# Kernel optimization log

Hardware: AMD Instinct MI355X
Metric: run time of the kernel (lower is better)

The kernel has to match this reference:

```python
import jax, jax.numpy as jnp
import numpy as np

D = 256; DFF = 1024; NH = 8; NL = 4; NP = 4; HD = D // NH
N = 8; LQ = 1024
SHAPES = np.array([[8, 64, 64], [8, 32, 32], [8, 16, 16], [8, 8, 8]], dtype=np.int32)
LIN = int(SHAPES.prod(axis=1).sum())  # 43520
LSI = np.concatenate([[0], np.cumsum(SHAPES.prod(axis=1))[:-1]]).astype(np.int32)


def setup_inputs() -> dict:
    key = jax.random.key(0)
    ks = jax.random.split(key, 16)
    s = 0.02
    inp = {
        "tgt": jax.random.normal(ks[0], (N, LQ, D), jnp.float32),
        "query_pos": jax.random.normal(ks[1], (N, LQ, D), jnp.float32),
        "reference_points": jax.random.uniform(ks[2], (N, LQ, NL, 3), jnp.float32),
        "src": jax.random.normal(ks[3], (N, LIN, D), jnp.float32),
        "src_spatio_temporal_shapes": jnp.asarray(SHAPES),
        "level_start_index": jnp.asarray(LSI),
        "src_padding_mask": jnp.zeros((N, LIN), dtype=bool),
        # MSDeformAttn3D params (weights stored (in,out) so y = x @ W + b)
        "value_proj_w": jax.random.normal(ks[4], (D, D), jnp.float32) * s,
        "value_proj_b": jnp.zeros((D,), jnp.float32),
        "samp_off_w": jax.random.normal(ks[5], (D, NH * NL * NP * 3), jnp.float32) * s,
        "samp_off_b": jax.random.normal(ks[6], (NH * NL * NP * 3,), jnp.float32) * s,
        "attn_w_w": jax.random.normal(ks[7], (D, NH * NL * NP), jnp.float32) * s,
        "attn_w_b": jnp.zeros((NH * NL * NP,), jnp.float32),
        "out_proj_w": jax.random.normal(ks[8], (D, D), jnp.float32) * s,
        "out_proj_b": jnp.zeros((D,), jnp.float32),
        # norm1 / FFN / norm3
        "ln1_g": jnp.ones((D,), jnp.float32),
        "ln1_b": jnp.zeros((D,), jnp.float32),
        "lin1_w": jax.random.normal(ks[9], (D, DFF), jnp.float32) * s,
        "lin1_b": jnp.zeros((DFF,), jnp.float32),
        "lin2_w": jax.random.normal(ks[10], (DFF, D), jnp.float32) * s,
        "lin2_b": jnp.zeros((D,), jnp.float32),
        "ln3_g": jnp.ones((D,), jnp.float32),
        "ln3_b": jnp.zeros((D,), jnp.float32),
    }
    return inp


def _ln(x, g, b, eps=1e-5):
    m = x.mean(-1, keepdims=True)
    v = x.var(-1, keepdims=True)
    return (x - m) / jnp.sqrt(v + eps) * g + b


def _ms_deform_attn3d(q, reference_points, src, shapes, lsi, pad_mask,
                      value_proj_w, value_proj_b, samp_off_w, samp_off_b,
                      attn_w_w, attn_w_b, out_proj_w, out_proj_b):
    n, lq, _ = q.shape
    value = src @ value_proj_w + value_proj_b                 # [N,Lin,D]
    value = jnp.where(pad_mask[:, :, None], 0.0, value)
    value = value.reshape(n, -1, NH, HD)                      # [N,Lin,H,hd]
    off = (q @ samp_off_w + samp_off_b).reshape(n, lq, NH, NL, NP, 3)
    aw = (q @ attn_w_w + attn_w_b).reshape(n, lq, NH, NL * NP)
    aw = jax.nn.softmax(aw, axis=-1).reshape(n, lq, NH, NL, NP)

    acc = jnp.zeros((n, lq, NH, HD), q.dtype)
    for l in range(NL):
        Tl, Hl, Wl = shapes[l, 0], shapes[l, 1], shapes[l, 2]
        sz = shapes[l].astype(q.dtype)                        # (T,H,W)
        start = lsi[l]
        # sampling locations in normalized (t,h,w) coords, [N,Lq,H,P,3]
        loc = reference_points[:, :, None, l, None, :] + off[:, :, :, l] / sz
        p = loc * sz - 0.5                                    # align_corners=False pixel coords
        p0 = jnp.floor(p)
        f = p - p0
        p0 = p0.astype(jnp.int32)
        samp = jnp.zeros((n, lq, NH, NP, HD), q.dtype)
        for dt in (0, 1):
            for dy in (0, 1):
                for dx in (0, 1):
                    it = p0[..., 0] + dt
                    iy = p0[..., 1] + dy
                    ix = p0[..., 2] + dx
                    w = ((f[..., 0] if dt else 1 - f[..., 0]) *
                         (f[..., 1] if dy else 1 - f[..., 1]) *
                         (f[..., 2] if dx else 1 - f[..., 2]))
                    valid = ((it >= 0) & (it < Tl) & (iy >= 0) & (iy < Hl) &
                             (ix >= 0) & (ix < Wl))
                    idx = start + (jnp.clip(it, 0, Tl - 1) * Hl +
                                   jnp.clip(iy, 0, Hl - 1)) * Wl + jnp.clip(ix, 0, Wl - 1)
                    # gather: idx [N,Lq,H,P] -> [N,Lq*P,H,1]
                    gi = idx.transpose(0, 1, 3, 2).reshape(n, lq * NP, NH, 1)
                    g = jnp.take_along_axis(value, gi, axis=1)
                    g = g.reshape(n, lq, NP, NH, HD).transpose(0, 1, 3, 2, 4)
                    samp = samp + (w * valid)[..., None] * g
        acc = acc + jnp.einsum('nqhp,nqhpd->nqhd', aw[:, :, :, l], samp)
    return acc.reshape(n, lq, D) @ out_proj_w + out_proj_b


def reference(tgt, query_pos, reference_points, src, src_spatio_temporal_shapes,
              level_start_index, src_padding_mask,
              value_proj_w, value_proj_b, samp_off_w, samp_off_b,
              attn_w_w, attn_w_b, out_proj_w, out_proj_b,
              ln1_g, ln1_b, lin1_w, lin1_b, lin2_w, lin2_b, ln3_g, ln3_b):
    q = tgt + query_pos
    tgt2 = _ms_deform_attn3d(q, reference_points, src, src_spatio_temporal_shapes,
                             level_start_index, src_padding_mask,
                             value_proj_w, value_proj_b, samp_off_w, samp_off_b,
                             attn_w_w, attn_w_b, out_proj_w, out_proj_b)
    x = _ln(tgt + tgt2, ln1_g, ln1_b)
    ff = jax.nn.relu(x @ lin1_w + lin1_b) @ lin2_w + lin2_b
    return _ln(x + ff, ln3_g, ln3_b)
```

## Files before the change

### kernel.cpp

```cpp
#include <hip/hip_runtime.h>

#define D_      256
#define DFF_    1024
#define NHEADS  8
#define NLVL    4
#define NPTS    4
#define HDIM    32
#define NBATCH  8
#define LQ_     1024
#define LIN_    43520
#define NQ_     (NBATCH * LQ_)
#define MV_     (NBATCH * LIN_)

typedef unsigned short u16;
typedef __attribute__((ext_vector_type(8))) short bf16x8;
typedef __attribute__((ext_vector_type(4))) float f32x4;

__device__ __forceinline__ u16 f2bf(float f) {
    unsigned u = __float_as_uint(f);
    return (u16)((u + 0x7FFFu + ((u >> 16) & 1u)) >> 16);
}
__device__ __forceinline__ float bf2f(u16 s) {
    return __uint_as_float(((unsigned)s) << 16);
}

template<bool OUT_BF16, bool RELU>
__global__ __launch_bounds__(256)
void gemm64(const float* __restrict__ A, const u16* __restrict__ Bt,
            const float* __restrict__ bias1, const float* __restrict__ bias2, int bsplit,
            const float* __restrict__ res,
            float* __restrict__ Cf, u16* __restrict__ Cb,
            int M, int N, int K)
{
    __shared__ u16 As[64][72];
    __shared__ u16 Bs[64][72];

    const int tid  = threadIdx.x;
    const int lane = tid & 63;
    const int w    = tid >> 6;
    const int wm   = w >> 1, wn = w & 1;
    const size_t m0 = (size_t)blockIdx.x * 64;
    const int    n0 = blockIdx.y * 64;
    const int r15 = lane & 15;
    const int kq  = lane >> 4;

    const f32x4 zero = {0.f, 0.f, 0.f, 0.f};
    f32x4 acc[2][2] = {{zero, zero}, {zero, zero}};

    for (int kt = 0; kt < K; kt += 64) {
        #pragma unroll
        for (int i = 0; i < 4; ++i) {
            int f   = tid + i * 256;
            int row = f >> 4;
            int c4  = f & 15;
            float4 v = *(const float4*)(A + (m0 + row) * K + kt + c4 * 4);
            unsigned lo = (unsigned)f2bf(v.x) | ((unsigned)f2bf(v.y) << 16);
            unsigned hi = (unsigned)f2bf(v.z) | ((unsigned)f2bf(v.w) << 16);
            *(uint2*)(&As[row][c4 * 4]) = make_uint2(lo, hi);
        }
        #pragma unroll
        for (int i = 0; i < 2; ++i) {
            int c  = tid + i * 256;
            int n  = c >> 3;
            int k8 = c & 7;
            uint4 v = *(const uint4*)(Bt + (size_t)(n0 + n) * K + kt + k8 * 8);
            *(uint4*)(&Bs[n][k8 * 8]) = v;
        }
        __syncthreads();

        #pragma unroll
        for (int kk = 0; kk < 2; ++kk) {
            int kb = kk * 32 + kq * 8;
            bf16x8 a0 = *(const bf16x8*)(&As[wm * 32 +      r15][kb]);
            bf16x8 a1 = *(const bf16x8*)(&As[wm * 32 + 16 + r15][kb]);
            bf16x8 b0 = *(const bf16x8*)(&Bs[wn * 32 +      r15][kb]);
            bf16x8 b1 = *(const bf16x8*)(&Bs[wn * 32 + 16 + r15][kb]);
            acc[0][0] = __builtin_amdgcn_mfma_f32_16x16x32_bf16(a0, b0, acc[0][0], 0, 0, 0);
            acc[0][1] = __builtin_amdgcn_mfma_f32_16x16x32_bf16(a0, b1, acc[0][1], 0, 0, 0);
            acc[1][0] = __builtin_amdgcn_mfma_f32_16x16x32_bf16(a1, b0, acc[1][0], 0, 0, 0);
            acc[1][1] = __builtin_amdgcn_mfma_f32_16x16x32_bf16(a1, b1, acc[1][1], 0, 0, 0);
        }
        __syncthreads();
    }

    #pragma unroll
    for (int fm = 0; fm < 2; ++fm) {
        #pragma unroll
        for (int fn = 0; fn < 2; ++fn) {
            int col = n0 + wn * 32 + fn * 16 + r15;
            float b = (bias2 != nullptr && col >= bsplit) ? bias2[col - bsplit] : bias1[col];
            #pragma unroll
            for (int j = 0; j < 4; ++j) {
                size_t row = m0 + wm * 32 + fm * 16 + kq * 4 + j;
                float v = acc[fm][fn][j] + b;
                if (res) v += res[row * N + col];
                if (RELU) v = fmaxf(v, 0.f);
                if (OUT_BF16) Cb[row * N + col] = f2bf(v);
                else          Cf[row * N + col] = v;
            }
        }
    }
}

__global__ void convT(const float* __restrict__ in, u16* __restrict__ out, int K, int N)
{
    int tid = blockIdx.x * 256 + threadIdx.x;
    if (tid >= K * N) return;
    int n = tid / K, k = tid - n * K;
    out[tid] = f2bf(in[(size_t)k * N + n]);
}

__global__ void add_vec(const float4* __restrict__ a, const float4* __restrict__ b,
                        float4* __restrict__ o, int n4)
{
    int i = blockIdx.x * 256 + threadIdx.x;
    if (i < n4) {
        float4 x = a[i], y = b[i];
        o[i] = make_float4(x.x + y.x, x.y + y.y, x.z + y.z, x.w + y.w);
    }
}

__global__ void softmax16(float* __restrict__ oa)
{
    int r = blockIdx.x * 256 + threadIdx.x;
    if (r >= NQ_ * NHEADS) return;
    int q = r >> 3, h = r & 7;
    float* p = oa + (size_t)q * 512 + 384 + h * 16;
    float m = -1e30f;
    #pragma unroll
    for (int i = 0; i < 16; ++i) m = fmaxf(m, p[i]);
    float e[16], s = 0.f;
    #pragma unroll
    for (int i = 0; i < 16; ++i) { e[i] = __expf(p[i] - m); s += e[i]; }
    float inv = 1.f / s;
    #pragma unroll
    for (int i = 0; i < 16; ++i) p[i] = e[i] * inv;
}

__global__ __launch_bounds__(256)
void sample_kernel(const float* __restrict__ refpts, const float* __restrict__ offaw,
                   const u16* __restrict__ value, float* __restrict__ out)
{
    __shared__ int   sIdx[128][8];
    __shared__ float sW[128][8];

    const int b = blockIdx.x;
    const int n = b >> 10;
    const int tid = threadIdx.x;

    const int shp[4][3] = {{8,64,64},{8,32,32},{8,16,16},{8,8,8}};
    const int lsi[4] = {0, 32768, 40960, 43008};

    if (tid < 128) {
        int h = tid >> 4;
        int l = (tid >> 2) & 3;
        int p = tid & 3;
        const float* rp  = refpts + ((size_t)b * 4 + l) * 3;
        const float* off = offaw + (size_t)b * 512 + ((h * 4 + l) * 4 + p) * 3;
        float aw = offaw[(size_t)b * 512 + 384 + h * 16 + l * 4 + p];
        int T = shp[l][0], H = shp[l][1], W = shp[l][2];
        float pt = rp[0] * T + off[0] - 0.5f;
        float ph = rp[1] * H + off[1] - 0.5f;
        float pw = rp[2] * W + off[2] - 0.5f;
        float flt = floorf(pt), flh = floorf(ph), flw = floorf(pw);
        float ft = pt - flt, fh = ph - flh, fw = pw - flw;
        int it0 = (int)flt, ih0 = (int)flh, iw0 = (int)flw;
        #pragma unroll
        for (int c = 0; c < 8; ++c) {
            int dt = (c >> 2) & 1, dy = (c >> 1) & 1, dx = c & 1;
            int it = it0 + dt, iy = ih0 + dy, ix = iw0 + dx;
            bool valid = (it >= 0) && (it < T) && (iy >= 0) && (iy < H) &&
                         (ix >= 0) && (ix < W);
            float wgt = (dt ? ft : 1.f - ft) * (dy ? fh : 1.f - fh) * (dx ? fw : 1.f - fw);
            int ict = min(max(it, 0), T - 1);
            int icy = min(max(iy, 0), H - 1);
            int icx = min(max(ix, 0), W - 1);
            sIdx[tid][c] = lsi[l] + (ict * H + icy) * W + icx;
            sW[tid][c]   = valid ? aw * wgt : 0.f;
        }
    }
    __syncthreads();

    const int h = tid >> 5, d = tid & 31;
    const u16* vb = value + ((size_t)n * LIN_ * 8 + h) * 32 + d;
    float acc = 0.f;
    #pragma unroll
    for (int lp = 0; lp < 16; ++lp) {
        int e = h * 16 + lp;
        #pragma unroll
        for (int c = 0; c < 8; ++c) {
            float wgt = sW[e][c];
            int idx   = sIdx[e][c];
            acc += wgt * bf2f(vb[(size_t)idx * 256]);
        }
    }
    out[(size_t)b * 256 + tid] = acc;
}

__global__ __launch_bounds__(256)
void ln_kernel(const float* __restrict__ in, const float* __restrict__ g,
               const float* __restrict__ bta, float* __restrict__ out)
{
    int row = blockIdx.x, t = threadIdx.x;
    float v = in[(size_t)row * 256 + t];
    float s = v, q2 = v * v;
    #pragma unroll
    for (int o = 1; o < 64; o <<= 1) {
        s  += __shfl_xor(s, o);
        q2 += __shfl_xor(q2, o);
    }
    __shared__ float ss[4], sq[4];
    int w = t >> 6;
    if ((t & 63) == 0) { ss[w] = s; sq[w] = q2; }
    __syncthreads();
    float S = ss[0] + ss[1] + ss[2] + ss[3];
    float Q = sq[0] + sq[1] + sq[2] + sq[3];
    float mean = S * (1.f / 256.f);
    float var  = Q * (1.f / 256.f) - mean * mean;
    float inv  = rsqrtf(var + 1e-5f);
    out[(size_t)row * 256 + t] = (v - mean) * inv * g[t] + bta[t];
}

extern "C" void kernel_launch(void* const* d_in, const int* in_sizes, int n_in,
                              void* d_out, int out_size, void* d_ws, size_t ws_size,
                              hipStream_t stream)
{
    const float* tgt   = (const float*)d_in[0];
    const float* qpos  = (const float*)d_in[1];
    const float* refp  = (const float*)d_in[2];
    const float* src   = (const float*)d_in[3];
    const float* Wv  = (const float*)d_in[7];
    const float* bv  = (const float*)d_in[8];
    const float* Ws  = (const float*)d_in[9];
    const float* bs  = (const float*)d_in[10];
    const float* Wa  = (const float*)d_in[11];
    const float* ba  = (const float*)d_in[12];
    const float* Wo  = (const float*)d_in[13];
    const float* bo  = (const float*)d_in[14];
    const float* g1  = (const float*)d_in[15];
    const float* b1  = (const float*)d_in[16];
    const float* W1  = (const float*)d_in[17];
    const float* bb1 = (const float*)d_in[18];
    const float* W2  = (const float*)d_in[19];
    const float* bb2 = (const float*)d_in[20];
    const float* g3  = (const float*)d_in[21];
    const float* b3  = (const float*)d_in[22];
    float* out = (float*)d_out;

    char* ws = (char*)d_ws;
    size_t o = 0;
    u16* val   = (u16*)(ws + o); o += (size_t)MV_ * 256 * 2;
    u16* WvT   = (u16*)(ws + o); o += 256 * 256 * 2;
    u16* WcT   = (u16*)(ws + o); o += 512 * 256 * 2;
    u16* WoT   = (u16*)(ws + o); o += 256 * 256 * 2;
    u16* W1T   = (u16*)(ws + o); o += 1024 * 256 * 2;
    u16* W2T   = (u16*)(ws + o); o += 256 * 1024 * 2;
    float* q   = (float*)(ws + o); o += (size_t)NQ_ * 256 * 4;
    float* oa  = (float*)(ws + o); o += (size_t)NQ_ * 512 * 4;
    float* acc = (float*)(ws + o); o += (size_t)NQ_ * 256 * 4;
    float* xp  = (float*)(ws + o); o += (size_t)NQ_ * 256 * 4;
    float* hb  = (float*)(ws + o); o += (size_t)NQ_ * 1024 * 4;
    (void)ws_size; (void)in_sizes; (void)n_in; (void)out_size;

    convT<<<(256 * 256 + 255) / 256, 256, 0, stream>>>(Wv, WvT, 256, 256);
    convT<<<(256 * 384 + 255) / 256, 256, 0, stream>>>(Ws, WcT, 256, 384);
    convT<<<(256 * 128 + 255) / 256, 256, 0, stream>>>(Wa, WcT + 384 * 256, 256, 128);
    convT<<<(256 * 256 + 255) / 256, 256, 0, stream>>>(Wo, WoT, 256, 256);
    convT<<<(256 * 1024 + 255) / 256, 256, 0, stream>>>(W1, W1T, 256, 1024);
    convT<<<(1024 * 256 + 255) / 256, 256, 0, stream>>>(W2, W2T, 1024, 256);

    add_vec<<<(NQ_ * 256 / 4 + 255) / 256, 256, 0, stream>>>(
        (const float4*)tgt, (const float4*)qpos, (float4*)q, NQ_ * 256 / 4);

    gemm64<true, false><<<dim3(MV_ / 64, 256 / 64), 256, 0, stream>>>(
        src, WvT, bv, nullptr, 1 << 30, nullptr, nullptr, val, MV_, 256, 256);

    gemm64<false, false><<<dim3(NQ_ / 64, 512 / 64), 256, 0, stream>>>(
        q, WcT, bs, ba, 384, nullptr, oa, nullptr, NQ_, 512, 256);

    softmax16<<<(NQ_ * NHEADS + 255) / 256, 256, 0, stream>>>(oa);

    sample_kernel<<<NQ_, 256, 0, stream>>>(refp, oa, val, acc);

    gemm64<false, false><<<dim3(NQ_ / 64, 256 / 64), 256, 0, stream>>>(
        acc, WoT, bo, nullptr, 1 << 30, tgt, xp, nullptr, NQ_, 256, 256);

    ln_kernel<<<NQ_, 256, 0, stream>>>(xp, g1, b1, q);

    gemm64<false, true><<<dim3(NQ_ / 64, 1024 / 64), 256, 0, stream>>>(
        q, W1T, bb1, nullptr, 1 << 30, nullptr, hb, nullptr, NQ_, 1024, 256);

    gemm64<false, false><<<dim3(NQ_ / 64, 256 / 64), 256, 0, stream>>>(
        hb, W2T, bb2, nullptr, 1 << 30, q, xp, nullptr, NQ_, 256, 1024);

    ln_kernel<<<NQ_, 256, 0, stream>>>(xp, g3, b3, out);
}
```

Measured before the change: 955.9 us.

## Widen GEMM N-tile to 256 so each A tile is converted once

The GEMM block tile grows from 64x64 to 64x256. Each wave now computes a 32x128 slice with 16 accumulators, and all launches shrink their grid's y dimension to match. Before, every fp32 A tile was reloaded and converted to bf16 once per 64-column block (up to 16 times for lin1). Now it is loaded once per 256 columns, which cuts redundant global reads and conversion work, especially for the large value projection over src. In exchange, each block uses more registers and LDS and the grid holds fewer blocks, which may reduce occupancy.

```diff
diff --git a/kernel.cpp b/kernel.cpp
--- a/kernel.cpp
+++ b/kernel.cpp
@@ -33,19 +33,23 @@
             int M, int N, int K)
 {
     __shared__ u16 As[64][72];
-    __shared__ u16 Bs[64][72];
+    __shared__ u16 Bs[256][72];
 
     const int tid  = threadIdx.x;
     const int lane = tid & 63;
     const int w    = tid >> 6;
     const int wm   = w >> 1, wn = w & 1;
     const size_t m0 = (size_t)blockIdx.x * 64;
-    const int    n0 = blockIdx.y * 64;
+    const int    n0 = blockIdx.y * 256;
     const int r15 = lane & 15;
     const int kq  = lane >> 4;
 
     const f32x4 zero = {0.f, 0.f, 0.f, 0.f};
-    f32x4 acc[2][2] = {{zero, zero}, {zero, zero}};
+    f32x4 acc[2][8];
+    #pragma unroll
+    for (int i = 0; i < 2; ++i)
+        #pragma unroll
+        for (int j = 0; j < 8; ++j) acc[i][j] = zero;
 
     for (int kt = 0; kt < K; kt += 64) {
         #pragma unroll
@@ -59,7 +63,7 @@
             *(uint2*)(&As[row][c4 * 4]) = make_uint2(lo, hi);
         }
         #pragma unroll
-        for (int i = 0; i < 2; ++i) {
+        for (int i = 0; i < 8; ++i) {
             int c  = tid + i * 256;
             int n  = c >> 3;
             int k8 = c & 7;
@@ -73,12 +77,15 @@
             int kb = kk * 32 + kq * 8;
             bf16x8 a0 = *(const bf16x8*)(&As[wm * 32 +      r15][kb]);
             bf16x8 a1 = *(const bf16x8*)(&As[wm * 32 + 16 + r15][kb]);
-            bf16x8 b0 = *(const bf16x8*)(&Bs[wn * 32 +      r15][kb]);
-            bf16x8 b1 = *(const bf16x8*)(&Bs[wn * 32 + 16 + r15][kb]);
-            acc[0][0] = __builtin_amdgcn_mfma_f32_16x16x32_bf16(a0, b0, acc[0][0], 0, 0, 0);
-            acc[0][1] = __builtin_amdgcn_mfma_f32_16x16x32_bf16(a0, b1, acc[0][1], 0, 0, 0);
-            acc[1][0] = __builtin_amdgcn_mfma_f32_16x16x32_bf16(a1, b0, acc[1][0], 0, 0, 0);
-            acc[1][1] = __builtin_amdgcn_mfma_f32_16x16x32_bf16(a1, b1, acc[1][1], 0, 0, 0);
+            bf16x8 bfr[8];
+            #pragma unroll
+            for (int fn = 0; fn < 8; ++fn)
+                bfr[fn] = *(const bf16x8*)(&Bs[wn * 128 + fn * 16 + r15][kb]);
+            #pragma unroll
+            for (int fn = 0; fn < 8; ++fn) {
+                acc[0][fn] = __builtin_amdgcn_mfma_f32_16x16x32_bf16(a0, bfr[fn], acc[0][fn], 0, 0, 0);
+                acc[1][fn] = __builtin_amdgcn_mfma_f32_16x16x32_bf16(a1, bfr[fn], acc[1][fn], 0, 0, 0);
+            }
         }
         __syncthreads();
     }
@@ -86,8 +93,8 @@
     #pragma unroll
     for (int fm = 0; fm < 2; ++fm) {
         #pragma unroll
-        for (int fn = 0; fn < 2; ++fn) {
-            int col = n0 + wn * 32 + fn * 16 + r15;
+        for (int fn = 0; fn < 8; ++fn) {
+            int col = n0 + wn * 128 + fn * 16 + r15;
             float b = (bias2 != nullptr && col >= bsplit) ? bias2[col - bsplit] : bias1[col];
             #pragma unroll
             for (int j = 0; j < 4; ++j) {
@@ -272,25 +279,25 @@
     add_vec<<<(NQ_ * 256 / 4 + 255) / 256, 256, 0, stream>>>(
         (const float4*)tgt, (const float4*)qpos, (float4*)q, NQ_ * 256 / 4);
 
-    gemm64<true, false><<<dim3(MV_ / 64, 256 / 64), 256, 0, stream>>>(
+    gemm64<true, false><<<dim3(MV_ / 64, 1), 256, 0, stream>>>(
         src, WvT, bv, nullptr, 1 << 30, nullptr, nullptr, val, MV_, 256, 256);
 
-    gemm64<false, false><<<dim3(NQ_ / 64, 512 / 64), 256, 0, stream>>>(
+    gemm64<false, false><<<dim3(NQ_ / 64, 2), 256, 0, stream>>>(
         q, WcT, bs, ba, 384, nullptr, oa, nullptr, NQ_, 512, 256);
 
     softmax16<<<(NQ_ * NHEADS + 255) / 256, 256, 0, stream>>>(oa);
 
     sample_kernel<<<NQ_, 256, 0, stream>>>(refp, oa, val, acc);
 
-    gemm64<false, false><<<dim3(NQ_ / 64, 256 / 64), 256, 0, stream>>>(
+    gemm64<false, false><<<dim3(NQ_ / 64, 1), 256, 0, stream>>>(
         acc, WoT, bo, nullptr, 1 << 30, tgt, xp, nullptr, NQ_, 256, 256);
 
     ln_kernel<<<NQ_, 256, 0, stream>>>(xp, g1, b1, q);
 
-    gemm64<false, true><<<dim3(NQ_ / 64, 1024 / 64), 256, 0, stream>>>(
+    gemm64<false, true><<<dim3(NQ_ / 64, 4), 256, 0, stream>>>(
         q, W1T, bb1, nullptr, 1 << 30, nullptr, hb, nullptr, NQ_, 1024, 256);
 
-    gemm64<false, false><<<dim3(NQ_ / 64, 256 / 64), 256, 0, stream>>>(
+    gemm64<false, false><<<dim3(NQ_ / 64, 1), 256, 0, stream>>>(
         hb, W2T, bb2, nullptr, 1 << 30, q, xp, nullptr, NQ_, 256, 1024);
 
     ln_kernel<<<NQ_, 256, 0, stream>>>(xp, g3, b3, out);
```

Measured after the change: 774.9 us. 18.9% less time.
